# Kernel tuning notes

Measured on AMD Instinct MI355X. Metric: run time of the kernel, lower is better.

Reference implementation:

```python
import math
import jax, jax.numpy as jnp
import numpy as np

B, T, C = 2, 2048, 1024
N_HEAD = 16
HEAD_DIM = C // N_HEAD


def setup_inputs() -> dict:
    key = jax.random.key(0)
    k1, k2, k3 = jax.random.split(key, 3)
    x = jax.random.normal(k1, (B, T, C), dtype=jnp.float32)
    w_attn = jax.random.normal(k2, (3 * C, C), dtype=jnp.float32) * 0.02
    w_proj = jax.random.normal(k3, (C, C), dtype=jnp.float32) * 0.02
    return {"x": x, "w_attn": w_attn, "w_proj": w_proj}


def _rope_cos_sin(seq_len, dim, dtype):
    inv_freq = 1.0 / (10000.0 ** (jnp.arange(0, dim, 2, dtype=jnp.float32) / dim))
    t = jnp.arange(seq_len, dtype=jnp.float32)
    freqs = jnp.einsum('i,j->ij', t, inv_freq)          # [T, dim/2]
    emb = jnp.concatenate([freqs, freqs], axis=-1)       # [T, dim]
    return jnp.cos(emb).astype(dtype), jnp.sin(emb).astype(dtype)


def _rotate_half(x):
    x1, x2 = jnp.split(x, 2, axis=-1)
    return jnp.concatenate([-x2, x1], axis=-1)


def _apply_rope(x, cos, sin):
    # x: [B, H, T, D]; cos/sin: [T, D] broadcast over batch/head
    return x * cos[None, None] + _rotate_half(x) * sin[None, None]


def reference(x, w_attn, w_proj):
    b, t, c = x.shape
    h, d = N_HEAD, c // N_HEAD
    qkv = x @ w_attn.T                                   # [B, T, 3C]
    q, k, v = jnp.split(qkv, 3, axis=-1)
    q = q.reshape(b, t, h, d).transpose(0, 2, 1, 3)      # [B, H, T, D]
    k = k.reshape(b, t, h, d).transpose(0, 2, 1, 3)
    v = v.reshape(b, t, h, d).transpose(0, 2, 1, 3)
    cos, sin = _rope_cos_sin(t, d, x.dtype)
    q = _apply_rope(q, cos, sin)
    k = _apply_rope(k, cos, sin)
    logits = jnp.einsum('bhqd,bhkd->bhqk', q, k) * (1.0 / math.sqrt(d))
    causal = jnp.tril(jnp.ones((t, t), dtype=bool))
    logits = jnp.where(causal[None, None], logits, jnp.float32(-jnp.inf).astype(logits.dtype))
    att = jax.nn.softmax(logits, axis=-1)                # [B, H, T, T]
    y = jnp.einsum('bhqk,bhkd->bhqd', att, v)            # [B, H, T, D]
    y = y.transpose(0, 2, 1, 3).reshape(b, t, c)
    return y @ w_proj.T
```

## Files before the change

### kernel.cpp

```cpp
#include <hip/hip_runtime.h>
#include <hip/hip_bf16.h>
#include <math.h>

#define B_ 2
#define T_ 2048
#define C_ 1024
#define H_ 16

typedef __bf16 bf16x8 __attribute__((ext_vector_type(8)));
typedef __bf16 bf16x4 __attribute__((ext_vector_type(4)));
typedef float f32x4 __attribute__((ext_vector_type(4)));
typedef float f32x16 __attribute__((ext_vector_type(16)));
typedef unsigned int u32;

#if __has_builtin(__builtin_amdgcn_exp2f)
#define EXP2(x) __builtin_amdgcn_exp2f(x)
#else
#define EXP2(x) exp2f(x)
#endif

__device__ __forceinline__ void gload16(const void* g, void* l) {
    __builtin_amdgcn_global_load_lds(
        (const __attribute__((address_space(1))) void*)g,
        (__attribute__((address_space(3))) void*)l, 16, 0, 0);
}

__device__ __forceinline__ f32x4 mfma16(bf16x8 a, bf16x8 b, f32x4 c) {
    return __builtin_amdgcn_mfma_f32_16x16x32_bf16(a, b, c, 0, 0, 0);
}
__device__ __forceinline__ f32x16 mfma32(bf16x8 a, bf16x8 b, f32x16 c) {
    return __builtin_amdgcn_mfma_f32_32x32x16_bf16(a, b, c, 0, 0, 0);
}

__device__ __forceinline__ u32 cvtpk(float lo, float hi) {
    u32 r;
    asm("v_cvt_pk_bf16_f32 %0, %1, %2" : "=v"(r) : "v"(lo), "v"(hi));
    return r;
}

__device__ __forceinline__ void plane32swap(u32& a, u32& b) {
#if __has_builtin(__builtin_amdgcn_permlane32_swap)
    auto r = __builtin_amdgcn_permlane32_swap(a, b, false, false);
    a = r[0]; b = r[1];
#else
    asm("v_permlane32_swap_b32 %0, %1" : "+v"(a), "+v"(b));
#endif
}

#define SCLQ 0.18033688011112042f
#define NLOG2_10K_32 (-0.4152410118609203f)

__global__ __launch_bounds__(256) void cast_all(const float* __restrict__ x,
                                                const float* __restrict__ wa,
                                                const float* __restrict__ wp,
                                                __bf16* __restrict__ xb,
                                                __bf16* __restrict__ wab,
                                                __bf16* __restrict__ wpb) {
    const int i = blockIdx.x * 256 + threadIdx.x;
    const float* src;
    __bf16* dst;
    int k;
    if (i < 1048576)               { src = x;  dst = xb;  k = i; }
    else if (i < 1048576 + 786432) { src = wa; dst = wab; k = i - 1048576; }
    else                           { src = wp; dst = wpb; k = i - (1048576 + 786432); }
    float4 v = ((const float4*)src)[k];
    bf16x4 o;
    o[0] = (__bf16)v.x; o[1] = (__bf16)v.y; o[2] = (__bf16)v.z; o[3] = (__bf16)v.w;
    ((bf16x4*)dst)[k] = o;
}

__global__ __launch_bounds__(256) void gemm_qkv(const __bf16* __restrict__ A,
                                                const __bf16* __restrict__ Bw,
                                                __bf16* __restrict__ Qb,
                                                __bf16* __restrict__ Kb,
                                                __bf16* __restrict__ Vt) {
    const int tid  = threadIdx.x;
    const int lane = tid & 63;
    const int w    = tid >> 6;
    const int wr = w >> 1, wc = w & 1;
    const int l15 = lane & 15, lg = lane >> 4;
    const int d0  = blockIdx.y * 24 + blockIdx.x;
    const int xcd = d0 & 7, kk0 = d0 >> 3;
    const int by  = xcd * 4 + (kk0 / 24);
    const int bx  = kk0 % 24;
    const int bm = by * 128, bn = bx * 128;
    const int K = C_;
    __shared__ __bf16 Asm[128 * 64];
    __shared__ __bf16 Bsm[128 * 64];
    f32x4 acc[4][4] = {};

    for (int kt = 0; kt < K; kt += 64) {
        if (kt) __syncthreads();
#pragma unroll
        for (int it = 0; it < 4; ++it) {
            const int c = it * 256 + tid;
            const int row = c >> 3, sg = (c & 7) ^ (row & 7);
            gload16(A  + (size_t)(bm + row) * K + kt + sg * 8, Asm + c * 8);
            gload16(Bw + (size_t)(bn + row) * K + kt + sg * 8, Bsm + c * 8);
        }
        __syncthreads();
#pragma unroll
        for (int k2 = 0; k2 < 2; ++k2) {
            bf16x8 af[4], bf[4];
#pragma unroll
            for (int i = 0; i < 4; ++i) {
                const int row = wr * 64 + i * 16 + l15;
                af[i] = *(const bf16x8*)&Asm[row * 64 + (((k2 * 4 + lg) ^ (row & 7)) * 8)];
            }
#pragma unroll
            for (int j = 0; j < 4; ++j) {
                const int row = wc * 64 + j * 16 + l15;
                bf[j] = *(const bf16x8*)&Bsm[row * 64 + (((k2 * 4 + lg) ^ (row & 7)) * 8)];
            }
#pragma unroll
            for (int i = 0; i < 4; ++i)
#pragma unroll
                for (int j = 0; j < 4; ++j)
                    acc[i][j] = mfma16(af[i], bf[j], acc[i][j]);
        }
    }
    const int region  = bn >> 10;
    const int colbase = (bn & 1023) + wc * 64;
    const int h = colbase >> 6;
    if (region < 2) {
        __bf16* dst = region ? Kb : Qb;
        const float scl = region ? 1.0f : SCLQ;
#pragma unroll
        for (int j = 0; j < 2; ++j) {
            const int d = j * 16 + l15;
            const float invf = exp2f((float)d * NLOG2_10K_32);
#pragma unroll
            for (int i = 0; i < 4; ++i)
#pragma unroll
                for (int r = 0; r < 4; ++r) {
                    const int row = bm + wr * 64 + i * 16 + lg * 4 + r;
                    const int b = row >> 11, t = row & (T_ - 1);
                    float sv, cv;
                    __sincosf((float)t * invf, &sv, &cv);
                    const float v1 = acc[i][j][r], v2 = acc[i][j + 2][r];
                    const float o1 = (v1 * cv - v2 * sv) * scl;
                    const float o2 = (v2 * cv + v1 * sv) * scl;
                    const size_t base = ((size_t)(b * H_ + h) * T_ + t) * 64;
                    dst[base + d]      = (__bf16)o1;
                    dst[base + d + 32] = (__bf16)o2;
                }
        }
    } else {
#pragma unroll
        for (int i = 0; i < 4; ++i)
#pragma unroll
            for (int j = 0; j < 4; ++j) {
                const int vcol = colbase + j * 16 + l15;
                const int hh = vcol >> 6, d = vcol & 63;
                const int row0 = bm + wr * 64 + i * 16 + lg * 4;
                const int b = row0 >> 11, t0 = row0 & (T_ - 1);
                u32 dw[2];
                dw[0] = cvtpk(acc[i][j][0], acc[i][j][1]);
                dw[1] = cvtpk(acc[i][j][2], acc[i][j][3]);
                *(uint64_t*)&Vt[((size_t)(b * H_ + hh) * 64 + d) * T_ + t0] =
                    *(uint64_t*)dw;
            }
    }
}

__global__ __launch_bounds__(256) void gemm_proj(const __bf16* __restrict__ A,
                                                 const __bf16* __restrict__ Bw,
                                                 float* __restrict__ Cp,
                                                 int N, int K) {
    const int tid  = threadIdx.x;
    const int lane = tid & 63;
    const int w    = tid >> 6;
    const int wr = w >> 1, wc = w & 1;
    const int l15 = lane & 15, lg = lane >> 4;
    const int d0  = blockIdx.y * 8 + blockIdx.x;
    const int xcd = d0 & 7, kk0 = d0 >> 3;
    const int by  = xcd * 8 + (kk0 >> 3);
    const int bx  = kk0 & 7;
    const int bm = by * 64, bn = bx * 128;
    __shared__ __bf16 Asm[64 * 64];
    __shared__ __bf16 Bsm[128 * 64];
    f32x4 acc[2][4] = {};

    for (int kt = 0; kt < K; kt += 64) {
        if (kt) __syncthreads();
#pragma unroll
        for (int it = 0; it < 2; ++it) {
            const int g = it * 256 + tid;
            const int row = g >> 3, sg = (g & 7) ^ (row & 7);
            gload16(A + (size_t)(bm + row) * K + kt + sg * 8, Asm + g * 8);
        }
#pragma unroll
        for (int it = 0; it < 4; ++it) {
            const int g = it * 256 + tid;
            const int row = g >> 3, sg = (g & 7) ^ (row & 7);
            gload16(Bw + (size_t)(bn + row) * K + kt + sg * 8, Bsm + g * 8);
        }
        __syncthreads();
#pragma unroll
        for (int k2 = 0; k2 < 2; ++k2) {
            bf16x8 af[2], bf[4];
#pragma unroll
            for (int i = 0; i < 2; ++i) {
                const int row = wr * 32 + i * 16 + l15;
                af[i] = *(const bf16x8*)&Asm[row * 64 + (((k2 * 4 + lg) ^ (row & 7)) * 8)];
            }
#pragma unroll
            for (int j = 0; j < 4; ++j) {
                const int row = wc * 64 + j * 16 + l15;
                bf[j] = *(const bf16x8*)&Bsm[row * 64 + (((k2 * 4 + lg) ^ (row & 7)) * 8)];
            }
#pragma unroll
            for (int i = 0; i < 2; ++i)
#pragma unroll
                for (int j = 0; j < 4; ++j)
                    acc[i][j] = mfma16(af[i], bf[j], acc[i][j]);
        }
    }
#pragma unroll
    for (int i = 0; i < 2; ++i)
#pragma unroll
        for (int j = 0; j < 4; ++j)
#pragma unroll
            for (int r = 0; r < 4; ++r) {
                const int row = bm + wr * 32 + i * 16 + lg * 4 + r;
                const int col = bn + wc * 64 + j * 16 + l15;
                Cp[(size_t)row * N + col] = acc[i][j][r];
            }
}

__global__ __launch_bounds__(512, 2) void attn_fwd(const __bf16* __restrict__ Qb,
                                                   const __bf16* __restrict__ Kb,
                                                   const __bf16* __restrict__ Vt,
                                                   __bf16* __restrict__ Yatt) {
    const int gid = blockIdx.x;
    const int bh = (gid & 7) * 4 + ((gid >> 3) & 3);
    const int qq = gid >> 5;
    const int qt = (qq < 8) ? (15 - qq) : (qq - 8);
    const int b = bh >> 4, h = bh & 15;
    const int tid = threadIdx.x, lane = tid & 63, w = tid >> 6;
    const int qgrp = w & 3, kvh = w >> 2;
    const int l31 = lane & 31, hi = lane >> 5;
    const int hi4 = hi * 4;
    __shared__ __bf16 Ksm[256 * 64];
    __shared__ __bf16 Vsm[64 * 256];

    const int Q0 = qt * 128 + qgrp * 32;
    const int qg = Q0 + l31;
    const __bf16* Qp = Qb + ((size_t)bh * T_ + Q0) * 64;
    const __bf16* Kp = Kb + (size_t)bh * T_ * 64;
    const __bf16* Vp = Vt + (size_t)bh * 64 * T_;

    auto STAGE = [&](int jt) {
#pragma unroll
        for (int it = 0; it < 4; ++it) {
            const int g = it * 512 + tid;
            const int kr = g >> 3, kc = (g & 7) ^ (kr & 7);
            gload16(Kp + ((size_t)(jt * 256 + kr)) * 64 + kc * 8, Ksm + g * 8);
            const int vd = g >> 5, vg = ((g & 15) ^ (vd & 15)) | (g & 16);
            gload16(Vp + (size_t)vd * T_ + jt * 256 + vg * 8, Vsm + g * 8);
        }
    };

    bf16x8 qf[4];
#pragma unroll
    for (int ds = 0; ds < 4; ++ds)
        qf[ds] = *(const bf16x8*)&Qp[l31 * 64 + ds * 16 + hi * 8];

    f32x16 ot[2] = {};
    float l_run = 0.f;

    const int jmax = (qt >> 1) + 1;
    for (int jt = 0; jt < jmax; ++jt) {
        __builtin_amdgcn_s_barrier();
        STAGE(jt);
        asm volatile("s_waitcnt vmcnt(0)" ::: "memory");
        __builtin_amdgcn_s_barrier();
        __builtin_amdgcn_sched_barrier(0);

        if (jt * 256 + kvh * 128 <= Q0 + 31) {
            const bool diag = (jt == jmax - 1);
#pragma unroll
            for (int a = 0; a < 4; ++a) {
                f32x16 st = {};
#pragma unroll
                for (int ds = 0; ds < 4; ++ds) {
                    const int row = kvh * 128 + a * 32 + l31;
                    const int off = (ds * 32 + hi * 16) ^ ((row & 7) << 4);
                    bf16x8 kf = *(const bf16x8*)((const char*)Ksm + row * 128 + off);
                    st = mfma32(kf, qf[ds], st);
                }
                if (diag) {
#pragma unroll
                    for (int r = 0; r < 16; ++r) {
                        const int kv = jt * 256 + kvh * 128 + a * 32 +
                                       (r & 3) + 8 * (r >> 2) + hi4;
                        if (kv > qg) st[r] = -1e30f;
                    }
                }
                float s0 = 0.f, s1 = 0.f;
#pragma unroll
                for (int r = 0; r < 16; ++r) {
                    const float e = EXP2(st[r]);
                    st[r] = e;
                    if (r & 1) s1 += e; else s0 += e;
                }
                l_run += s0 + s1;
                u32 X0 = cvtpk(st[0], st[1]),  X1 = cvtpk(st[2], st[3]);
                u32 Y0 = cvtpk(st[4], st[5]),  Y1 = cvtpk(st[6], st[7]);
                plane32swap(X0, Y0); plane32swap(X1, Y1);
                u32 dw0[4] = {X0, X1, Y0, Y1};
                bf16x8 pa0 = *(bf16x8*)dw0;
                u32 Z0 = cvtpk(st[8], st[9]),   Z1 = cvtpk(st[10], st[11]);
                u32 W0 = cvtpk(st[12], st[13]), W1 = cvtpk(st[14], st[15]);
                plane32swap(Z0, W0); plane32swap(Z1, W1);
                u32 dw1[4] = {Z0, Z1, W0, W1};
                bf16x8 pa1 = *(bf16x8*)dw1;
#pragma unroll
                for (int db = 0; db < 2; ++db) {
                    const int row = db * 32 + l31;
                    const int g0 = (kvh * 16) | ((4 * a + hi)     ^ (row & 15));
                    const int g1 = (kvh * 16) | ((4 * a + 2 + hi) ^ (row & 15));
                    bf16x8 v0 = *(const bf16x8*)((const char*)Vsm + row * 512 + g0 * 16);
                    bf16x8 v1 = *(const bf16x8*)((const char*)Vsm + row * 512 + g1 * 16);
                    ot[db] = mfma32(v0, pa0, ot[db]);
                    ot[db] = mfma32(v1, pa1, ot[db]);
                }
            }
        }
    }
    __builtin_amdgcn_s_barrier();
    f32x4* m4 = (f32x4*)&Ksm[0];
    float* lb = (float*)&Vsm[0];
    if (w >= 4) {
        const int woff = (w - 4) * 64 + lane;
#pragma unroll
        for (int db = 0; db < 2; ++db)
#pragma unroll
            for (int rq = 0; rq < 4; ++rq) {
                f32x4 v;
                v[0] = ot[db][rq * 4 + 0]; v[1] = ot[db][rq * 4 + 1];
                v[2] = ot[db][rq * 4 + 2]; v[3] = ot[db][rq * 4 + 3];
                m4[(db * 4 + rq) * 256 + woff] = v;
            }
        lb[woff] = l_run;
    }
    __builtin_amdgcn_s_barrier();
    if (w < 4) {
        const int woff = w * 64 + lane;
#pragma unroll
        for (int db = 0; db < 2; ++db)
#pragma unroll
            for (int rq = 0; rq < 4; ++rq) {
                f32x4 v = m4[(db * 4 + rq) * 256 + woff];
                ot[db][rq * 4 + 0] += v[0]; ot[db][rq * 4 + 1] += v[1];
                ot[db][rq * 4 + 2] += v[2]; ot[db][rq * 4 + 3] += v[3];
            }
        l_run += lb[woff];
        l_run += __shfl_xor(l_run, 32);
        const float inv = 1.f / l_run;
        __bf16* Yp = Yatt + ((size_t)(b * T_ + qg)) * C_ + h * 64;
#pragma unroll
        for (int db = 0; db < 2; ++db)
#pragma unroll
            for (int rq = 0; rq < 4; ++rq) {
                const int r = rq * 4;
                u32 dw[2];
                dw[0] = cvtpk(ot[db][r] * inv,     ot[db][r + 1] * inv);
                dw[1] = cvtpk(ot[db][r + 2] * inv, ot[db][r + 3] * inv);
                const int d = db * 32 + 8 * rq + hi4;
                *(uint64_t*)&Yp[d] = *(uint64_t*)dw;
            }
    }
}

extern "C" void kernel_launch(void* const* d_in, const int* in_sizes, int n_in,
                              void* d_out, int out_size, void* d_ws, size_t ws_size,
                              hipStream_t stream) {
    const float* x      = (const float*)d_in[0];
    const float* w_attn = (const float*)d_in[1];
    const float* w_proj = (const float*)d_in[2];
    float* out = (float*)d_out;
    char* ws = (char*)d_ws;

    __bf16* xb  = (__bf16*)(ws);
    __bf16* wab = (__bf16*)(ws + 8388608);
    __bf16* wpb = (__bf16*)(ws + 14680064);
    __bf16* Qb  = (__bf16*)(ws + 16777216);
    __bf16* Kb  = (__bf16*)(ws + 25165824);
    __bf16* Vt  = (__bf16*)(ws + 33554432);
    __bf16* Ya  = (__bf16*)(ws + 41943040);

    cast_all<<<dim3(8192), 256, 0, stream>>>(x, w_attn, w_proj, xb, wab, wpb);

    gemm_qkv<<<dim3(3 * C_ / 128, B_ * T_ / 128), 256, 0, stream>>>(
        xb, wab, Qb, Kb, Vt);

    attn_fwd<<<dim3(16 * 32), 512, 0, stream>>>(Qb, Kb, Vt, Ya);

    gemm_proj<<<dim3(C_ / 128, B_ * T_ / 64), 256, 0, stream>>>(
        Ya, wpb, out, C_, C_);
}
```

Before: 97.10 us.

## Overlap V tile load with QK^T and softmax by splitting the wait

Splits the K/V staging into separate K and V loads and waits only on the K loads (vmcnt(4)) before computing QK^T and the exp for all four sub-tiles. The probabilities are buffered in registers, then a second wait and barrier cover the V loads before the PV MFMAs run. This hides V-tile global load latency behind score computation, at the cost of an extra barrier per iteration and more live registers for the buffered P fragments.

Result: no change. 97.76 us (+0.7%).

```diff
diff --git a/kernel.cpp b/kernel.cpp
--- a/kernel.cpp
+++ b/kernel.cpp
@@ -250,12 +250,18 @@
     const __bf16* Kp = Kb + (size_t)bh * T_ * 64;
     const __bf16* Vp = Vt + (size_t)bh * 64 * T_;
 
-    auto STAGE = [&](int jt) {
+    auto STAGE_K = [&](int jt) {
 #pragma unroll
         for (int it = 0; it < 4; ++it) {
             const int g = it * 512 + tid;
             const int kr = g >> 3, kc = (g & 7) ^ (kr & 7);
             gload16(Kp + ((size_t)(jt * 256 + kr)) * 64 + kc * 8, Ksm + g * 8);
+        }
+    };
+    auto STAGE_V = [&](int jt) {
+#pragma unroll
+        for (int it = 0; it < 4; ++it) {
+            const int g = it * 512 + tid;
             const int vd = g >> 5, vg = ((g & 15) ^ (vd & 15)) | (g & 16);
             gload16(Vp + (size_t)vd * T_ + jt * 256 + vg * 8, Vsm + g * 8);
         }
@@ -272,13 +278,16 @@
     const int jmax = (qt >> 1) + 1;
     for (int jt = 0; jt < jmax; ++jt) {
         __builtin_amdgcn_s_barrier();
-        STAGE(jt);
-        asm volatile("s_waitcnt vmcnt(0)" ::: "memory");
+        STAGE_K(jt);
+        STAGE_V(jt);
+        asm volatile("s_waitcnt vmcnt(4)" ::: "memory");
         __builtin_amdgcn_s_barrier();
         __builtin_amdgcn_sched_barrier(0);
 
-        if (jt * 256 + kvh * 128 <= Q0 + 31) {
-            const bool diag = (jt == jmax - 1);
+        const bool work = (jt * 256 + kvh * 128 <= Q0 + 31);
+        const bool diag = (jt == jmax - 1);
+        bf16x8 pa[4][2];
+        if (work) {
 #pragma unroll
             for (int a = 0; a < 4; ++a) {
                 f32x16 st = {};
@@ -309,12 +318,20 @@
                 u32 Y0 = cvtpk(st[4], st[5]),  Y1 = cvtpk(st[6], st[7]);
                 plane32swap(X0, Y0); plane32swap(X1, Y1);
                 u32 dw0[4] = {X0, X1, Y0, Y1};
-                bf16x8 pa0 = *(bf16x8*)dw0;
+                pa[a][0] = *(bf16x8*)dw0;
                 u32 Z0 = cvtpk(st[8], st[9]),   Z1 = cvtpk(st[10], st[11]);
                 u32 W0 = cvtpk(st[12], st[13]), W1 = cvtpk(st[14], st[15]);
                 plane32swap(Z0, W0); plane32swap(Z1, W1);
                 u32 dw1[4] = {Z0, Z1, W0, W1};
-                bf16x8 pa1 = *(bf16x8*)dw1;
+                pa[a][1] = *(bf16x8*)dw1;
+            }
+        }
+        asm volatile("s_waitcnt vmcnt(0)" ::: "memory");
+        __builtin_amdgcn_s_barrier();
+        __builtin_amdgcn_sched_barrier(0);
+        if (work) {
+#pragma unroll
+            for (int a = 0; a < 4; ++a)
 #pragma unroll
                 for (int db = 0; db < 2; ++db) {
                     const int row = db * 32 + l31;
@@ -322,10 +339,9 @@
                     const int g1 = (kvh * 16) | ((4 * a + 2 + hi) ^ (row & 15));
                     bf16x8 v0 = *(const bf16x8*)((const char*)Vsm + row * 512 + g0 * 16);
                     bf16x8 v1 = *(const bf16x8*)((const char*)Vsm + row * 512 + g1 * 16);
-                    ot[db] = mfma32(v0, pa0, ot[db]);
-                    ot[db] = mfma32(v1, pa1, ot[db]);
+                    ot[db] = mfma32(v0, pa[a][0], ot[db]);
+                    ot[db] = mfma32(v1, pa[a][1], ot[db]);
                 }
-            }
         }
     }
     __builtin_amdgcn_s_barrier();
```
